# Optimization experiments

Measured on AMD Instinct MI355X. Metric: run time of the kernel, lower is better.

The kernel has to match this reference:

```python
import jax, jax.numpy as jnp
import numpy as np

N_NODES = 50000
N_EDGES = 800000
IN_CH = 256
HID = 32
HEADS1 = 4
OUT_CH = 64
NEG_SLOPE = 0.2


def setup_inputs() -> dict:
    key = jax.random.key(0)
    ks = jax.random.split(key, 10)
    x = jax.random.normal(ks[0], (N_NODES, IN_CH), dtype=jnp.float32)
    edge_index = jax.random.randint(ks[1], (2, N_EDGES), 0, N_NODES, dtype=jnp.int64)
    g1 = float(np.sqrt(2.0 / (IN_CH + HEADS1 * HID)))
    g2 = float(np.sqrt(2.0 / (HEADS1 * HID + OUT_CH)))
    return {
        "x": x,
        "edge_index": edge_index,
        "W1": jax.random.normal(ks[2], (IN_CH, HEADS1 * HID), dtype=jnp.float32) * g1,
        "a_src1": jax.random.normal(ks[3], (HEADS1, HID), dtype=jnp.float32) * 0.1,
        "a_dst1": jax.random.normal(ks[4], (HEADS1, HID), dtype=jnp.float32) * 0.1,
        "b1": jnp.zeros((HEADS1 * HID,), dtype=jnp.float32),
        "W2": jax.random.normal(ks[5], (HEADS1 * HID, OUT_CH), dtype=jnp.float32) * g2,
        "a_src2": jax.random.normal(ks[6], (1, OUT_CH), dtype=jnp.float32) * 0.1,
        "a_dst2": jax.random.normal(ks[7], (1, OUT_CH), dtype=jnp.float32) * 0.1,
        "b2": jnp.zeros((OUT_CH,), dtype=jnp.float32),
    }


def gat_conv(x, src, dst, W, a_s, a_d, b, concat):
    # PyG-style GATConv: per-head linear, additive attention, edge softmax over dst,
    # scatter-add aggregation.
    N = x.shape[0]
    H, C = a_s.shape
    h = (x @ W).reshape(N, H, C)                    # [N, H, C]
    as_n = jnp.einsum("nhc,hc->nh", h, a_s)         # [N, H]
    ad_n = jnp.einsum("nhc,hc->nh", h, a_d)         # [N, H]
    e = jax.nn.leaky_relu(as_n[src] + ad_n[dst], NEG_SLOPE)  # [E, H]
    # segment softmax over incoming edges of each dst node
    m = jax.lax.stop_gradient(jax.ops.segment_max(e, dst, num_segments=N))
    ex = jnp.exp(e - m[dst])
    denom = jax.ops.segment_sum(ex, dst, num_segments=N)
    alpha = ex / (denom[dst] + 1e-16)               # [E, H]
    msg = h[src] * alpha[:, :, None]                # [E, H, C]
    out = jax.ops.segment_sum(msg, dst, num_segments=N)  # [N, H, C]
    out = out.reshape(N, H * C) if concat else out.mean(axis=1)
    return out + b


def reference(x, edge_index, W1, a_src1, a_dst1, b1, W2, a_src2, a_dst2, b2):
    # eval mode: dropout(p=0.5) is identity
    src, dst = edge_index[0], edge_index[1]
    h = gat_conv(x, src, dst, W1, a_src1, a_dst1, b1, concat=True)
    h = jax.nn.relu(h)
    return gat_conv(h, src, dst, W2, a_src2, a_dst2, b2, concat=False)
```

## Files before the change

### kernel.cpp

```cpp
#include <hip/hip_runtime.h>
#include <hip/hip_fp16.h>

#define N_NODES 50000
#define N_EDGES 800000
#define IN_CH   256
#define HID     32
#define HEADS1  4
#define C1      128
#define OUT_CH  64
#define NEG     0.2f
#define INVLN2  1.4426950408889634f
#define BSHIFT  10
#define NBKT    49
#define BCAP    17664

typedef _Float16 h8 __attribute__((ext_vector_type(8)));
typedef _Float16 h4 __attribute__((ext_vector_type(4)));
typedef float f32x4 __attribute__((ext_vector_type(4)));

__global__ void k_prep(const float* __restrict__ W1, const float* __restrict__ W2,
                       _Float16* __restrict__ Wt1, _Float16* __restrict__ Wt2,
                       int* __restrict__ bcur) {
    int t = blockIdx.x * 256 + threadIdx.x;
    if (blockIdx.x == 0 && threadIdx.x < NBKT) bcur[threadIdx.x] = threadIdx.x * BCAP;
    if (t < C1 * IN_CH) {
        int c = t >> 8, k = t & 255;
        Wt1[t] = (_Float16)W1[(size_t)k * C1 + c];
    }
    if (t < OUT_CH * C1) {
        int c = t >> 7, k = t & 127;
        Wt2[t] = (_Float16)W2[(size_t)k * OUT_CH + c];
    }
}

__global__ __launch_bounds__(256) void gemm1_mfma(const float* __restrict__ X,
                                                  const _Float16* __restrict__ Wt1,
                                                  const float* __restrict__ a_s1,
                                                  const float* __restrict__ a_d1,
                                                  __half* __restrict__ H,
                                                  float* __restrict__ as_n,
                                                  float* __restrict__ ad_n) {
    __shared__ _Float16 As[64 * 40];
    __shared__ _Float16 Bt[128 * 40];
    const int tid = threadIdx.x;
    const int w = tid >> 6, lane = tid & 63;
    const int row0 = blockIdx.x * 64;
    const int lr = lane & 15, lk = (lane >> 4) * 8;
    f32x4 acc[8];
#pragma unroll
    for (int n = 0; n < 8; ++n) acc[n] = (f32x4){0.f, 0.f, 0.f, 0.f};

    for (int kk = 0; kk < IN_CH; kk += 32) {
        {
            int ar = tid >> 2, aks = (tid & 3) * 8;
            int gr = row0 + ar;
            float4 v0 = make_float4(0.f, 0.f, 0.f, 0.f), v1 = v0;
            if (gr < N_NODES) {
                v0 = *(const float4*)(X + (size_t)gr * IN_CH + kk + aks);
                v1 = *(const float4*)(X + (size_t)gr * IN_CH + kk + aks + 4);
            }
            h8 hv;
            hv[0] = (_Float16)v0.x; hv[1] = (_Float16)v0.y;
            hv[2] = (_Float16)v0.z; hv[3] = (_Float16)v0.w;
            hv[4] = (_Float16)v1.x; hv[5] = (_Float16)v1.y;
            hv[6] = (_Float16)v1.z; hv[7] = (_Float16)v1.w;
            *(h8*)(&As[ar * 40 + aks]) = hv;
        }
        {
            int c = tid >> 1, q = tid & 1;
            const h8* wp = (const h8*)(Wt1 + (size_t)c * IN_CH + kk + q * 16);
            *(h8*)(&Bt[c * 40 + q * 16]) = wp[0];
            *(h8*)(&Bt[c * 40 + q * 16 + 8]) = wp[1];
        }
        __syncthreads();
        h8 a = *(const h8*)(&As[(w * 16 + lr) * 40 + lk]);
#pragma unroll
        for (int n = 0; n < 8; ++n) {
            h8 b = *(const h8*)(&Bt[(n * 16 + lr) * 40 + lk]);
            acc[n] = __builtin_amdgcn_mfma_f32_16x16x32_f16(a, b, acc[n], 0, 0, 0);
        }
        __syncthreads();
    }
#pragma unroll
    for (int n = 0; n < 8; ++n)
#pragma unroll
        for (int j = 0; j < 4; ++j) {
            int gr = row0 + w * 16 + (lane >> 4) * 4 + j;
            if (gr < N_NODES) H[(size_t)gr * C1 + n * 16 + lr] = __float2half(acc[n][j]);
        }
    float sa0[4], sa1[4], da0[4], da1[4];
#pragma unroll
    for (int h = 0; h < 4; ++h) {
        sa0[h] = a_s1[h * 32 + lr] * INVLN2;
        sa1[h] = a_s1[h * 32 + 16 + lr] * INVLN2;
        da0[h] = a_d1[h * 32 + lr] * INVLN2;
        da1[h] = a_d1[h * 32 + 16 + lr] * INVLN2;
    }
#pragma unroll
    for (int j = 0; j < 4; ++j) {
        float sv[4], dv[4];
#pragma unroll
        for (int h = 0; h < 4; ++h) {
            sv[h] = fmaf(acc[2 * h][j], sa0[h], acc[2 * h + 1][j] * sa1[h]);
            dv[h] = fmaf(acc[2 * h][j], da0[h], acc[2 * h + 1][j] * da1[h]);
        }
#pragma unroll
        for (int m = 1; m <= 8; m <<= 1)
#pragma unroll
            for (int h = 0; h < 4; ++h) {
                sv[h] += __shfl_xor(sv[h], m);
                dv[h] += __shfl_xor(dv[h], m);
            }
        int gr = row0 + w * 16 + (lane >> 4) * 4 + j;
        if (lr == 0 && gr < N_NODES) {
#pragma unroll
            for (int h = 0; h < 4; ++h) {
                as_n[gr * 4 + h] = sv[h];
                ad_n[gr * 4 + h] = dv[h];
            }
        }
    }
}

__global__ __launch_bounds__(256) void gemm2_mfma(const __half* __restrict__ A,
                                                  const _Float16* __restrict__ Wt2,
                                                  const float* __restrict__ a_s2,
                                                  const float* __restrict__ a_d2,
                                                  __half* __restrict__ H,
                                                  float* __restrict__ as_n,
                                                  float* __restrict__ ad_n) {
    __shared__ _Float16 Bt[64 * 136];
    const int tid = threadIdx.x;
    const int w = tid >> 6, lane = tid & 63;
    const int row0 = blockIdx.x * 64;
    const int lr = lane & 15, lk = (lane >> 4) * 8;
    {
        int c = tid >> 2, q = tid & 3;
        const h8* wp = (const h8*)(Wt2 + (size_t)c * C1 + q * 32);
#pragma unroll
        for (int j = 0; j < 4; ++j)
            *(h8*)(&Bt[c * 136 + q * 32 + j * 8]) = wp[j];
    }
    __syncthreads();
    f32x4 acc[4];
#pragma unroll
    for (int n = 0; n < 4; ++n) acc[n] = (f32x4){0.f, 0.f, 0.f, 0.f};
    int grow = row0 + w * 16 + lr;
    grow = grow < N_NODES ? grow : N_NODES - 1;
    const _Float16* Ah = (const _Float16*)A;
#pragma unroll
    for (int kk = 0; kk < C1; kk += 32) {
        h8 a = *(const h8*)(Ah + (size_t)grow * C1 + kk + lk);
#pragma unroll
        for (int n = 0; n < 4; ++n) {
            h8 b = *(const h8*)(&Bt[(n * 16 + lr) * 136 + kk + lk]);
            acc[n] = __builtin_amdgcn_mfma_f32_16x16x32_f16(a, b, acc[n], 0, 0, 0);
        }
    }
#pragma unroll
    for (int n = 0; n < 4; ++n)
#pragma unroll
        for (int j = 0; j < 4; ++j) {
            int gr = row0 + w * 16 + (lane >> 4) * 4 + j;
            if (gr < N_NODES) H[(size_t)gr * OUT_CH + n * 16 + lr] = __float2half(acc[n][j]);
        }
    float sa[4], da[4];
#pragma unroll
    for (int n = 0; n < 4; ++n) {
        sa[n] = a_s2[n * 16 + lr] * INVLN2;
        da[n] = a_d2[n * 16 + lr] * INVLN2;
    }
#pragma unroll
    for (int j = 0; j < 4; ++j) {
        float sv = 0.f, dv = 0.f;
#pragma unroll
        for (int n = 0; n < 4; ++n) {
            sv = fmaf(acc[n][j], sa[n], sv);
            dv = fmaf(acc[n][j], da[n], dv);
        }
#pragma unroll
        for (int m = 1; m <= 8; m <<= 1) {
            sv += __shfl_xor(sv, m);
            dv += __shfl_xor(dv, m);
        }
        int gr = row0 + w * 16 + (lane >> 4) * 4 + j;
        if (lr == 0 && gr < N_NODES) {
            as_n[gr] = sv;
            ad_n[gr] = dv;
        }
    }
}

__global__ __launch_bounds__(256) void k_bucket(const int* __restrict__ src,
                                                const int* __restrict__ dst,
                                                int* __restrict__ bcur,
                                                int* __restrict__ pairs) {
    __shared__ int cnt[NBKT];
    __shared__ int base[NBKT];
    const int t = threadIdx.x;
    if (t < NBKT) cnt[t] = 0;
    __syncthreads();
    const int e0 = blockIdx.x * 2048;
    int s[8], d[8], r[8];
#pragma unroll
    for (int k = 0; k < 8; ++k) {
        int e = e0 + t + k * 256;
        bool v = e < N_EDGES;
        s[k] = v ? src[e] : 0;
        d[k] = v ? dst[e] : -1;
        r[k] = v ? atomicAdd(&cnt[d[k] >> BSHIFT], 1) : 0;
    }
    __syncthreads();
    if (t < NBKT) base[t] = atomicAdd(&bcur[t], cnt[t]);
    __syncthreads();
#pragma unroll
    for (int k = 0; k < 8; ++k) {
        if (d[k] >= 0) {
            int bin = d[k] >> BSHIFT;
            int pos = base[bin] + r[k];
            if (pos < (bin + 1) * BCAP)
                pairs[pos] = ((d[k] & 1023) << 16) | s[k];
        }
    }
}

__global__ __launch_bounds__(256) void k_csr(const int* __restrict__ pairs,
                                             const int* __restrict__ bcur,
                                             int* __restrict__ estart,
                                             int* __restrict__ eend,
                                             int* __restrict__ esrc) {
    __shared__ int hist[1024];
    __shared__ int cur[1024];
    __shared__ int s[256];
    const int b = blockIdx.x;
    const int t = threadIdx.x;
#pragma unroll
    for (int k = t; k < 1024; k += 256) hist[k] = 0;
    __syncthreads();
    int cnt = bcur[b] - b * BCAP;
    if (cnt > BCAP) cnt = BCAP;
    const int* p = pairs + (size_t)b * BCAP;
    for (int i = t; i < cnt; i += 256)
        atomicAdd(&hist[p[i] >> 16], 1);
    __syncthreads();
    int h0 = hist[4 * t], h1 = hist[4 * t + 1], h2 = hist[4 * t + 2], h3 = hist[4 * t + 3];
    int sum = h0 + h1 + h2 + h3;
    s[t] = sum;
    __syncthreads();
#pragma unroll
    for (int o = 1; o < 256; o <<= 1) {
        int v = (t >= o) ? s[t - o] : 0;
        __syncthreads();
        s[t] += v;
        __syncthreads();
    }
    int excl = s[t] - sum;
    int gbase = b * BCAP + excl;
    cur[4 * t]     = gbase;
    cur[4 * t + 1] = gbase + h0;
    cur[4 * t + 2] = gbase + h0 + h1;
    cur[4 * t + 3] = gbase + h0 + h1 + h2;
    const int nbase = b << BSHIFT;
#pragma unroll
    for (int i = 0; i < 4; ++i) {
        int node = nbase + 4 * t + i;
        if (node < N_NODES) {
            int st = cur[4 * t + i];
            estart[node] = st;
            eend[node] = st + hist[4 * t + i];
        }
    }
    __syncthreads();
    for (int i = t; i < cnt; i += 256) {
        int v = p[i];
        int pos = atomicAdd(&cur[v >> 16], 1);
        esrc[pos] = v & 0xFFFF;
    }
}

__global__ __launch_bounds__(256) void gat_aggr1_csr(const int* __restrict__ estart,
                                                     const int* __restrict__ eend,
                                                     const int* __restrict__ esrc,
                                                     const float* __restrict__ as1,
                                                     const float* __restrict__ ad1,
                                                     const __half* __restrict__ h1,
                                                     const float* __restrict__ b1,
                                                     __half* __restrict__ hrelu) {
    int n = blockIdx.x * 4 + (threadIdx.x >> 6);
    if (n >= N_NODES) return;
    const int lane = threadIdx.x & 63;
    const int q = lane >> 4, li = lane & 15;
    const int head = li >> 2;
    const int c0 = li * 8;
    const int base = estart[n];
    const int end = eend[n];
    const float ad = ad1[n * 4 + head];
    const _Float16* __restrict__ H = (const _Float16*)h1;
    float den0 = 0.f, den1 = 0.f;
    float acc0[8], acc1[8];
#pragma unroll
    for (int k = 0; k < 8; ++k) { acc0[k] = 0.f; acc1[k] = 0.f; }

    for (int b0 = base; b0 < end; b0 += 64) {
        int cnt = end - b0; if (cnt > 64) cnt = 64;
        int myidx = (lane < cnt) ? esrc[b0 + lane] : 0;
        for (int it = 0; it < cnt; it += 8) {
            int j0 = it + q * 2, j1 = j0 + 1;
            bool p0 = j0 < cnt, p1 = j1 < cnt;
            int s0 = __shfl(myidx, p0 ? j0 : 0);
            int s1 = __shfl(myidx, p1 ? j1 : 0);
            float x0 = as1[s0 * 4 + head] + ad;
            x0 = x0 > 0.f ? x0 : NEG * x0;
            float w0 = p0 ? exp2f(x0) : 0.f;
            float x1 = as1[s1 * 4 + head] + ad;
            x1 = x1 > 0.f ? x1 : NEG * x1;
            float w1 = p1 ? exp2f(x1) : 0.f;
            h8 hv0 = *(const h8*)(H + (size_t)s0 * C1 + c0);
            h8 hv1 = *(const h8*)(H + (size_t)s1 * C1 + c0);
            den0 += w0;
            den1 += w1;
#pragma unroll
            for (int k = 0; k < 8; ++k) {
                acc0[k] = fmaf((float)hv0[k], w0, acc0[k]);
                acc1[k] = fmaf((float)hv1[k], w1, acc1[k]);
            }
        }
    }
    float den = den0 + den1;
    float r[8];
#pragma unroll
    for (int k = 0; k < 8; ++k) r[k] = acc0[k] + acc1[k];
    den += __shfl_xor(den, 16);
    den += __shfl_xor(den, 32);
#pragma unroll
    for (int k = 0; k < 8; ++k) {
        r[k] += __shfl_xor(r[k], 16);
        r[k] += __shfl_xor(r[k], 32);
    }
    if (q == 0) {
        float4 bb0 = *(const float4*)(b1 + c0);
        float4 bb1 = *(const float4*)(b1 + c0 + 4);
        float bv[8] = {bb0.x, bb0.y, bb0.z, bb0.w, bb1.x, bb1.y, bb1.z, bb1.w};
        float inv = 1.f / (den + 1e-16f);
        h8 o;
#pragma unroll
        for (int k = 0; k < 8; ++k) {
            float v = fmaf(r[k], inv, bv[k]);
            o[k] = (_Float16)(v > 0.f ? v : 0.f);
        }
        *(h8*)((_Float16*)hrelu + (size_t)n * C1 + c0) = o;
    }
}

__global__ __launch_bounds__(256) void gat_aggr2_csr(const int* __restrict__ estart,
                                                     const int* __restrict__ eend,
                                                     const int* __restrict__ esrc,
                                                     const float* __restrict__ as2,
                                                     const float* __restrict__ ad2,
                                                     const __half* __restrict__ h2,
                                                     const float* __restrict__ b2,
                                                     float* __restrict__ out) {
    int n = blockIdx.x * 4 + (threadIdx.x >> 6);
    if (n >= N_NODES) return;
    const int lane = threadIdx.x & 63;
    const int q = lane >> 3, li = lane & 7;
    const int c0 = li * 8;
    const int base = estart[n];
    const int end = eend[n];
    const float ad = ad2[n];
    const _Float16* __restrict__ H = (const _Float16*)h2;
    float den0 = 0.f, den1 = 0.f;
    float acc0[8], acc1[8];
#pragma unroll
    for (int k = 0; k < 8; ++k) { acc0[k] = 0.f; acc1[k] = 0.f; }

    for (int b0 = base; b0 < end; b0 += 64) {
        int cnt = end - b0; if (cnt > 64) cnt = 64;
        int myidx = (lane < cnt) ? esrc[b0 + lane] : 0;
        for (int it = 0; it < cnt; it += 16) {
            int j0 = it + q * 2, j1 = j0 + 1;
            bool p0 = j0 < cnt, p1 = j1 < cnt;
            int s0 = __shfl(myidx, p0 ? j0 : 0);
            int s1 = __shfl(myidx, p1 ? j1 : 0);
            float x0 = as2[s0] + ad;
            x0 = x0 > 0.f ? x0 : NEG * x0;
            float w0 = p0 ? exp2f(x0) : 0.f;
            float x1 = as2[s1] + ad;
            x1 = x1 > 0.f ? x1 : NEG * x1;
            float w1 = p1 ? exp2f(x1) : 0.f;
            h8 hv0 = *(const h8*)(H + (size_t)s0 * OUT_CH + c0);
            h8 hv1 = *(const h8*)(H + (size_t)s1 * OUT_CH + c0);
            den0 += w0;
            den1 += w1;
#pragma unroll
            for (int k = 0; k < 8; ++k) {
                acc0[k] = fmaf((float)hv0[k], w0, acc0[k]);
                acc1[k] = fmaf((float)hv1[k], w1, acc1[k]);
            }
        }
    }
    float den = den0 + den1;
    float r[8];
#pragma unroll
    for (int k = 0; k < 8; ++k) r[k] = acc0[k] + acc1[k];
    den += __shfl_xor(den, 8);
    den += __shfl_xor(den, 16);
    den += __shfl_xor(den, 32);
#pragma unroll
    for (int k = 0; k < 8; ++k) {
        r[k] += __shfl_xor(r[k], 8);
        r[k] += __shfl_xor(r[k], 16);
        r[k] += __shfl_xor(r[k], 32);
    }
    if (q == 0) {
        float4 bb0 = *(const float4*)(b2 + c0);
        float4 bb1 = *(const float4*)(b2 + c0 + 4);
        float inv = 1.f / (den + 1e-16f);
        float4 o0, o1;
        o0.x = fmaf(r[0], inv, bb0.x);
        o0.y = fmaf(r[1], inv, bb0.y);
        o0.z = fmaf(r[2], inv, bb0.z);
        o0.w = fmaf(r[3], inv, bb0.w);
        o1.x = fmaf(r[4], inv, bb1.x);
        o1.y = fmaf(r[5], inv, bb1.y);
        o1.z = fmaf(r[6], inv, bb1.z);
        o1.w = fmaf(r[7], inv, bb1.w);
        *(float4*)(out + (size_t)n * OUT_CH + c0) = o0;
        *(float4*)(out + (size_t)n * OUT_CH + c0 + 4) = o1;
    }
}

extern "C" void kernel_launch(void* const* d_in, const int* in_sizes, int n_in,
                              void* d_out, int out_size, void* d_ws, size_t ws_size,
                              hipStream_t stream) {
    const float* x      = (const float*)d_in[0];
    const int*   ei     = (const int*)d_in[1];
    const float* W1     = (const float*)d_in[2];
    const float* a_src1 = (const float*)d_in[3];
    const float* a_dst1 = (const float*)d_in[4];
    const float* b1     = (const float*)d_in[5];
    const float* W2     = (const float*)d_in[6];
    const float* a_src2 = (const float*)d_in[7];
    const float* a_dst2 = (const float*)d_in[8];
    const float* b2     = (const float*)d_in[9];
    float* out = (float*)d_out;

    const int* src = ei;
    const int* dst = ei + N_EDGES;

    char* w = (char*)d_ws;
    auto carve = [&](size_t bytes) {
        char* p = w;
        w += (bytes + 255) & ~(size_t)255;
        return p;
    };
    __half*   h1     = (__half*)carve((size_t)N_NODES * C1 * 2);
    __half*   hrelu  = (__half*)carve((size_t)N_NODES * C1 * 2);
    float*    as1    = (float*)carve((size_t)N_NODES * 4 * 4);
    float*    ad1    = (float*)carve((size_t)N_NODES * 4 * 4);
    int*      estart = (int*)carve((size_t)N_NODES * 4);
    int*      eend   = (int*)carve((size_t)N_NODES * 4);
    int*      esrc   = (int*)carve((size_t)NBKT * BCAP * 4);
    int*      bcur   = (int*)carve((size_t)NBKT * 4);
    int*      pairs  = (int*)carve((size_t)NBKT * BCAP * 4);
    _Float16* Wt1    = (_Float16*)carve((size_t)C1 * IN_CH * 2);
    _Float16* Wt2    = (_Float16*)carve((size_t)OUT_CH * C1 * 2);

    __half* h2  = h1;
    float*  as2 = as1;
    float*  ad2 = ad1;

    k_prep<<<(C1 * IN_CH + 255) / 256, 256, 0, stream>>>(W1, W2, Wt1, Wt2, bcur);
    k_bucket<<<(N_EDGES + 2047) / 2048, 256, 0, stream>>>(src, dst, bcur, pairs);
    k_csr<<<NBKT, 256, 0, stream>>>(pairs, bcur, estart, eend, esrc);

    gemm1_mfma<<<(N_NODES + 63) / 64, 256, 0, stream>>>(x, Wt1, a_src1, a_dst1, h1, as1, ad1);
    gat_aggr1_csr<<<(N_NODES + 3) / 4, 256, 0, stream>>>(estart, eend, esrc, as1, ad1, h1, b1, hrelu);

    gemm2_mfma<<<(N_NODES + 63) / 64, 256, 0, stream>>>(hrelu, Wt2, a_src2, a_dst2, h2, as2, ad2);
    gat_aggr2_csr<<<(N_NODES + 3) / 4, 256, 0, stream>>>(estart, eend, esrc, as2, ad2, h2, b2, out);

    (void)in_sizes; (void)n_in; (void)out_size; (void)ws_size;
}
```

Before: 159.8 us.

## Fold attention vectors into weight matrices as extra GEMM output columns

Precomputes W·a_src and W·a_dst as extra columns appended to the transposed fp16 weight matrices in the prep kernel. The attention logits then come out of the MFMA GEMMs as an extra 16-wide tile, replacing the per-row FMA and shuffle reductions in the epilogue. This adds one MFMA tile per GEMM and more weight staging, and folding the attention vectors into fp16 weights changes rounding.

```diff
diff --git a/kernel.cpp b/kernel.cpp
--- a/kernel.cpp
+++ b/kernel.cpp
@@ -13,42 +13,67 @@
 #define BSHIFT  10
 #define NBKT    49
 #define BCAP    17664
+#define N1E     144
+#define N2E     80
 
 typedef _Float16 h8 __attribute__((ext_vector_type(8)));
-typedef _Float16 h4 __attribute__((ext_vector_type(4)));
 typedef float f32x4 __attribute__((ext_vector_type(4)));
 
 __global__ void k_prep(const float* __restrict__ W1, const float* __restrict__ W2,
-                       _Float16* __restrict__ Wt1, _Float16* __restrict__ Wt2,
+                       const float* __restrict__ a_s1, const float* __restrict__ a_d1,
+                       const float* __restrict__ a_s2, const float* __restrict__ a_d2,
+                       _Float16* __restrict__ Wt1e, _Float16* __restrict__ Wt2e,
                        int* __restrict__ bcur) {
     int t = blockIdx.x * 256 + threadIdx.x;
     if (blockIdx.x == 0 && threadIdx.x < NBKT) bcur[threadIdx.x] = threadIdx.x * BCAP;
-    if (t < C1 * IN_CH) {
+    if (t < 32768) {
         int c = t >> 8, k = t & 255;
-        Wt1[t] = (_Float16)W1[(size_t)k * C1 + c];
-    }
-    if (t < OUT_CH * C1) {
-        int c = t >> 7, k = t & 127;
-        Wt2[t] = (_Float16)W2[(size_t)k * OUT_CH + c];
+        Wt1e[(size_t)c * 256 + k] = (_Float16)W1[(size_t)k * C1 + c];
+    } else if (t < 34816) {
+        int i = t - 32768;
+        int k = i & 255, h = (i >> 8) & 3, which = i >> 10;
+        const float* av = which ? a_d1 : a_s1;
+        float s = 0.f;
+        for (int c = 0; c < 32; ++c)
+            s = fmaf(W1[(size_t)k * C1 + h * 32 + c], av[h * 32 + c], s);
+        Wt1e[(size_t)(128 + which * 4 + h) * 256 + k] = (_Float16)(s * INVLN2);
+    } else if (t < 36864) {
+        int i = t - 34816;
+        int k = i & 255, c = 136 + (i >> 8);
+        Wt1e[(size_t)c * 256 + k] = (_Float16)0.f;
+    } else if (t < 45056) {
+        int i = t - 36864;
+        int c = i >> 7, k = i & 127;
+        Wt2e[(size_t)c * 128 + k] = (_Float16)W2[(size_t)k * OUT_CH + c];
+    } else if (t < 45312) {
+        int i = t - 45056;
+        int k = i & 127, which = i >> 7;
+        const float* av = which ? a_d2 : a_s2;
+        float s = 0.f;
+        for (int c = 0; c < 64; ++c)
+            s = fmaf(W2[(size_t)k * OUT_CH + c], av[c], s);
+        Wt2e[(size_t)(64 + which) * 128 + k] = (_Float16)(s * INVLN2);
+    } else if (t < 47104) {
+        int i = t - 45312;
+        int k = i & 127, c = 66 + (i >> 7);
+        Wt2e[(size_t)c * 128 + k] = (_Float16)0.f;
     }
 }
 
 __global__ __launch_bounds__(256) void gemm1_mfma(const float* __restrict__ X,
-                                                  const _Float16* __restrict__ Wt1,
-                                                  const float* __restrict__ a_s1,
-                                                  const float* __restrict__ a_d1,
+                                                  const _Float16* __restrict__ Wt1e,
                                                   __half* __restrict__ H,
                                                   float* __restrict__ as_n,
                                                   float* __restrict__ ad_n) {
     __shared__ _Float16 As[64 * 40];
-    __shared__ _Float16 Bt[128 * 40];
+    __shared__ _Float16 Bt[N1E * 40];
     const int tid = threadIdx.x;
     const int w = tid >> 6, lane = tid & 63;
     const int row0 = blockIdx.x * 64;
     const int lr = lane & 15, lk = (lane >> 4) * 8;
-    f32x4 acc[8];
-#pragma unroll
-    for (int n = 0; n < 8; ++n) acc[n] = (f32x4){0.f, 0.f, 0.f, 0.f};
+    f32x4 acc[9];
+#pragma unroll
+    for (int n = 0; n < 9; ++n) acc[n] = (f32x4){0.f, 0.f, 0.f, 0.f};
 
     for (int kk = 0; kk < IN_CH; kk += 32) {
         {
@@ -66,16 +91,17 @@
             hv[6] = (_Float16)v1.z; hv[7] = (_Float16)v1.w;
             *(h8*)(&As[ar * 40 + aks]) = hv;
         }
-        {
-            int c = tid >> 1, q = tid & 1;
-            const h8* wp = (const h8*)(Wt1 + (size_t)c * IN_CH + kk + q * 16);
-            *(h8*)(&Bt[c * 40 + q * 16]) = wp[0];
-            *(h8*)(&Bt[c * 40 + q * 16 + 8]) = wp[1];
+        if (tid < N1E) {
+            const h8* wp = (const h8*)(Wt1e + (size_t)tid * IN_CH + kk);
+            *(h8*)(&Bt[tid * 40 + 0])  = wp[0];
+            *(h8*)(&Bt[tid * 40 + 8])  = wp[1];
+            *(h8*)(&Bt[tid * 40 + 16]) = wp[2];
+            *(h8*)(&Bt[tid * 40 + 24]) = wp[3];
         }
         __syncthreads();
         h8 a = *(const h8*)(&As[(w * 16 + lr) * 40 + lk]);
 #pragma unroll
-        for (int n = 0; n < 8; ++n) {
+        for (int n = 0; n < 9; ++n) {
             h8 b = *(const h8*)(&Bt[(n * 16 + lr) * 40 + lk]);
             acc[n] = __builtin_amdgcn_mfma_f32_16x16x32_f16(a, b, acc[n], 0, 0, 0);
         }
@@ -88,63 +114,37 @@
             int gr = row0 + w * 16 + (lane >> 4) * 4 + j;
             if (gr < N_NODES) H[(size_t)gr * C1 + n * 16 + lr] = __float2half(acc[n][j]);
         }
-    float sa0[4], sa1[4], da0[4], da1[4];
-#pragma unroll
-    for (int h = 0; h < 4; ++h) {
-        sa0[h] = a_s1[h * 32 + lr] * INVLN2;
-        sa1[h] = a_s1[h * 32 + 16 + lr] * INVLN2;
-        da0[h] = a_d1[h * 32 + lr] * INVLN2;
-        da1[h] = a_d1[h * 32 + 16 + lr] * INVLN2;
-    }
 #pragma unroll
     for (int j = 0; j < 4; ++j) {
-        float sv[4], dv[4];
-#pragma unroll
-        for (int h = 0; h < 4; ++h) {
-            sv[h] = fmaf(acc[2 * h][j], sa0[h], acc[2 * h + 1][j] * sa1[h]);
-            dv[h] = fmaf(acc[2 * h][j], da0[h], acc[2 * h + 1][j] * da1[h]);
-        }
-#pragma unroll
-        for (int m = 1; m <= 8; m <<= 1)
-#pragma unroll
-            for (int h = 0; h < 4; ++h) {
-                sv[h] += __shfl_xor(sv[h], m);
-                dv[h] += __shfl_xor(dv[h], m);
-            }
         int gr = row0 + w * 16 + (lane >> 4) * 4 + j;
-        if (lr == 0 && gr < N_NODES) {
-#pragma unroll
-            for (int h = 0; h < 4; ++h) {
-                as_n[gr * 4 + h] = sv[h];
-                ad_n[gr * 4 + h] = dv[h];
-            }
+        if (gr < N_NODES) {
+            if (lr < 4) as_n[gr * 4 + lr] = acc[8][j];
+            else if (lr < 8) ad_n[gr * 4 + (lr - 4)] = acc[8][j];
         }
     }
 }
 
 __global__ __launch_bounds__(256) void gemm2_mfma(const __half* __restrict__ A,
-                                                  const _Float16* __restrict__ Wt2,
-                                                  const float* __restrict__ a_s2,
-                                                  const float* __restrict__ a_d2,
+                                                  const _Float16* __restrict__ Wt2e,
                                                   __half* __restrict__ H,
                                                   float* __restrict__ as_n,
                                                   float* __restrict__ ad_n) {
-    __shared__ _Float16 Bt[64 * 136];
+    __shared__ _Float16 Bt[N2E * 136];
     const int tid = threadIdx.x;
     const int w = tid >> 6, lane = tid & 63;
     const int row0 = blockIdx.x * 64;
     const int lr = lane & 15, lk = (lane >> 4) * 8;
-    {
-        int c = tid >> 2, q = tid & 3;
-        const h8* wp = (const h8*)(Wt2 + (size_t)c * C1 + q * 32);
-#pragma unroll
-        for (int j = 0; j < 4; ++j)
-            *(h8*)(&Bt[c * 136 + q * 32 + j * 8]) = wp[j];
-    }
-    __syncthreads();
-    f32x4 acc[4];
-#pragma unroll
-    for (int n = 0; n < 4; ++n) acc[n] = (f32x4){0.f, 0.f, 0.f, 0.f};
+    if (tid < 160) {
+        int c = tid >> 1, q = tid & 1;
+        const h8* wp = (const h8*)(Wt2e + (size_t)c * C1 + q * 64);
+#pragma unroll
+        for (int j = 0; j < 8; ++j)
+            *(h8*)(&Bt[c * 136 + q * 64 + j * 8]) = wp[j];
+    }
+    __syncthreads();
+    f32x4 acc[5];
+#pragma unroll
+    for (int n = 0; n < 5; ++n) acc[n] = (f32x4){0.f, 0.f, 0.f, 0.f};
     int grow = row0 + w * 16 + lr;
     grow = grow < N_NODES ? grow : N_NODES - 1;
     const _Float16* Ah = (const _Float16*)A;
@@ -152,7 +152,7 @@
     for (int kk = 0; kk < C1; kk += 32) {
         h8 a = *(const h8*)(Ah + (size_t)grow * C1 + kk + lk);
 #pragma unroll
-        for (int n = 0; n < 4; ++n) {
+        for (int n = 0; n < 5; ++n) {
             h8 b = *(const h8*)(&Bt[(n * 16 + lr) * 136 + kk + lk]);
             acc[n] = __builtin_amdgcn_mfma_f32_16x16x32_f16(a, b, acc[n], 0, 0, 0);
         }
@@ -164,29 +164,12 @@
             int gr = row0 + w * 16 + (lane >> 4) * 4 + j;
             if (gr < N_NODES) H[(size_t)gr * OUT_CH + n * 16 + lr] = __float2half(acc[n][j]);
         }
-    float sa[4], da[4];
-#pragma unroll
-    for (int n = 0; n < 4; ++n) {
-        sa[n] = a_s2[n * 16 + lr] * INVLN2;
-        da[n] = a_d2[n * 16 + lr] * INVLN2;
-    }
 #pragma unroll
     for (int j = 0; j < 4; ++j) {
-        float sv = 0.f, dv = 0.f;
-#pragma unroll
-        for (int n = 0; n < 4; ++n) {
-            sv = fmaf(acc[n][j], sa[n], sv);
-            dv = fmaf(acc[n][j], da[n], dv);
-        }
-#pragma unroll
-        for (int m = 1; m <= 8; m <<= 1) {
-            sv += __shfl_xor(sv, m);
-            dv += __shfl_xor(dv, m);
-        }
         int gr = row0 + w * 16 + (lane >> 4) * 4 + j;
-        if (lr == 0 && gr < N_NODES) {
-            as_n[gr] = sv;
-            ad_n[gr] = dv;
+        if (gr < N_NODES) {
+            if (lr == 0) as_n[gr] = acc[4][j];
+            else if (lr == 1) ad_n[gr] = acc[4][j];
         }
     }
 }
@@ -463,21 +446,22 @@
     int*      esrc   = (int*)carve((size_t)NBKT * BCAP * 4);
     int*      bcur   = (int*)carve((size_t)NBKT * 4);
     int*      pairs  = (int*)carve((size_t)NBKT * BCAP * 4);
-    _Float16* Wt1    = (_Float16*)carve((size_t)C1 * IN_CH * 2);
-    _Float16* Wt2    = (_Float16*)carve((size_t)OUT_CH * C1 * 2);
+    _Float16* Wt1e   = (_Float16*)carve((size_t)N1E * IN_CH * 2);
+    _Float16* Wt2e   = (_Float16*)carve((size_t)N2E * C1 * 2);
 
     __half* h2  = h1;
     float*  as2 = as1;
     float*  ad2 = ad1;
 
-    k_prep<<<(C1 * IN_CH + 255) / 256, 256, 0, stream>>>(W1, W2, Wt1, Wt2, bcur);
+    k_prep<<<184, 256, 0, stream>>>(W1, W2, a_src1, a_dst1, a_src2, a_dst2,
+                                    Wt1e, Wt2e, bcur);
     k_bucket<<<(N_EDGES + 2047) / 2048, 256, 0, stream>>>(src, dst, bcur, pairs);
     k_csr<<<NBKT, 256, 0, stream>>>(pairs, bcur, estart, eend, esrc);
 
-    gemm1_mfma<<<(N_NODES + 63) / 64, 256, 0, stream>>>(x, Wt1, a_src1, a_dst1, h1, as1, ad1);
+    gemm1_mfma<<<(N_NODES + 63) / 64, 256, 0, stream>>>(x, Wt1e, h1, as1, ad1);
     gat_aggr1_csr<<<(N_NODES + 3) / 4, 256, 0, stream>>>(estart, eend, esrc, as1, ad1, h1, b1, hrelu);
 
-    gemm2_mfma<<<(N_NODES + 63) / 64, 256, 0, stream>>>(hrelu, Wt2, a_src2, a_dst2, h2, as2, ad2);
+    gemm2_mfma<<<(N_NODES + 63) / 64, 256, 0, stream>>>(hrelu, Wt2e, h2, as2, ad2);
     gat_aggr2_csr<<<(N_NODES + 3) / 4, 256, 0, stream>>>(estart, eend, esrc, as2, ad2, h2, b2, out);
 
     (void)in_sizes; (void)n_in; (void)out_size; (void)ws_size;
```

Measured after the change: 156.3 us. 1.02x faster.
